# Kernel optimization log

Measured on AMD Instinct MI355X. Metric: run time of the kernel, lower is better.

## Reference

```python
import jax, jax.numpy as jnp
import numpy as np

FEAT_DIM = 64   # C
EMBED_DIM = 64  # E
NUM_HEADS = 4
B, K, H, W = 4, 8, 128, 128


def setup_inputs() -> dict:
    key = jax.random.key(0)
    ks = jax.random.split(key, 24)
    C, E = FEAT_DIM, EMBED_DIM

    def lin_w(k, out_d, in_d):
        return jax.random.normal(k, (out_d, in_d), jnp.float32) * (1.0 / np.sqrt(in_d))

    def lin_b(k, out_d):
        return jax.random.normal(k, (out_d,), jnp.float32) * 0.01

    return {
        "HF_star": jax.random.normal(ks[0], (B, C, H, W), jnp.float32),
        "HF_cands": jax.random.normal(ks[1], (B, K, C, H, W), jnp.float32),
        "Z_cands": jax.random.normal(ks[2], (B, K, C, H, W), jnp.float32),
        "q1_w": lin_w(ks[3], E, C + 2), "q1_b": lin_b(ks[4], E),
        "k1_w": lin_w(ks[5], E, C + 2), "k1_b": lin_b(ks[6], E),
        "v1_w": lin_w(ks[7], E, C), "v1_b": lin_b(ks[8], E),
        "q2_w": lin_w(ks[9], E, C + E + 2), "q2_b": lin_b(ks[10], E),
        "k2_w": lin_w(ks[11], E, C + E + 2), "k2_b": lin_b(ks[12], E),
        "v2_w": lin_w(ks[13], E, C + E), "v2_b": lin_b(ks[14], E),
        "in_proj_w": lin_w(ks[15], 3 * E, E), "in_proj_b": lin_b(ks[16], 3 * E),
        "out_w": lin_w(ks[17], E, E), "out_b": lin_b(ks[18], E),
    }


def _mha(q, k, v, in_proj_w, in_proj_b, out_w, out_b, num_heads):
    # Replicates torch nn.MultiheadAttention with query len 1 per pixel.
    # q: [BN, E], k/v: [BN, K, E]
    E = q.shape[-1]
    d = E // num_heads
    wq, wk, wv = jnp.split(in_proj_w, 3, axis=0)
    bq, bk, bv = jnp.split(in_proj_b, 3, axis=0)
    qh = (q @ wq.T + bq).reshape(-1, num_heads, d)                  # [BN,h,d]
    kh = (k @ wk.T + bk).reshape(k.shape[0], k.shape[1], num_heads, d)  # [BN,K,h,d]
    vh = (v @ wv.T + bv).reshape(v.shape[0], v.shape[1], num_heads, d)
    scale = 1.0 / np.sqrt(d).astype(np.float32)
    scores = jnp.einsum('bhd,bkhd->bhk', qh, kh) * scale            # [BN,h,K]
    attn = jax.nn.softmax(scores, axis=-1)
    out = jnp.einsum('bhk,bkhd->bhd', attn, vh).reshape(-1, E)      # [BN,E]
    return out @ out_w.T + out_b


def reference(HF_star, HF_cands, Z_cands,
              q1_w, q1_b, k1_w, k1_b, v1_w, v1_b,
              q2_w, q2_b, k2_w, k2_b, v2_w, v2_b,
              in_proj_w, in_proj_b, out_w, out_b):
    Bb, C, Hh, Ww = HF_star.shape
    Kk = HF_cands.shape[1]
    N = Hh * Ww
    E = out_w.shape[0]

    i = jnp.linspace(0.0, 1.0, Hh)
    j = jnp.linspace(0.0, 1.0, Ww)
    ig, jg = jnp.meshgrid(i, j, indexing='ij')
    coords = jnp.stack([ig, jg], axis=-1)                            # [H,W,2]

    Qpix = jnp.transpose(HF_star, (0, 2, 3, 1))                      # [B,H,W,C]
    Kc = jnp.transpose(HF_cands, (0, 1, 3, 4, 2))                    # [B,K,H,W,C]
    Vc = jnp.transpose(Z_cands, (0, 1, 3, 4, 2))                     # [B,K,H,W,C]
    coords_q = jnp.broadcast_to(coords, (Bb, Hh, Ww, 2))
    coords_k = jnp.broadcast_to(coords, (Bb, Kk, Hh, Ww, 2))

    # Stage 1 (note: key reshape [B,K,H,W,D] -> [B*N,K,D] matches torch reshape semantics)
    Q1 = jnp.concatenate([Qpix, coords_q], axis=-1).reshape(Bb * N, C + 2)
    K1 = jnp.concatenate([Kc, coords_k], axis=-1).reshape(Bb * N, Kk, C + 2)
    V1 = Vc.reshape(Bb * N, Kk, C)
    q = Q1 @ q1_w.T + q1_b
    k = K1 @ k1_w.T + k1_b
    v = V1 @ v1_w.T + v1_b
    z_star = _mha(q, k, v, in_proj_w, in_proj_b, out_w, out_b, NUM_HEADS)
    z_bhwe = z_star.reshape(Bb, Hh, Ww, E)                           # [B,H,W,E]
    z_k = jnp.broadcast_to(z_bhwe[:, None], (Bb, Kk, Hh, Ww, E))

    # Stage 2
    Q2 = jnp.concatenate([Qpix, z_bhwe, coords_q], axis=-1).reshape(Bb * N, C + E + 2)
    K2 = jnp.concatenate([Kc, z_k, coords_k], axis=-1).reshape(Bb * N, Kk, C + E + 2)
    V2 = jnp.concatenate([Vc, z_k], axis=-1).reshape(Bb * N, Kk, C + E)
    q = Q2 @ q2_w.T + q2_b
    k = K2 @ k2_w.T + k2_b
    v = V2 @ v2_w.T + v2_b
    z_hat = _mha(q, k, v, in_proj_w, in_proj_b, out_w, out_b, NUM_HEADS)
    return jnp.transpose(z_hat.reshape(Bb, Hh, Ww, E), (0, 3, 1, 2))  # [B,E,H,W]
```

## Files before the change

### kernel.cpp

```cpp
#include <hip/hip_runtime.h>
#include <math.h>

#define HWp 16384
#define CH 64
#define KC 8
#define WSTRIDE 136

typedef __attribute__((ext_vector_type(8))) short bf16x8;
typedef __attribute__((ext_vector_type(4))) float f32x4;

#define MFMA(a, b, c) __builtin_amdgcn_mfma_f32_16x16x32_bf16(a, b, c, 0, 0, 0)

__device__ __forceinline__ short f2bf(float f) {
  unsigned u = __float_as_uint(f);
  u += 0x7FFFu + ((u >> 16) & 1u);
  return (short)(u >> 16);
}
__device__ __forceinline__ float bf2f(short s) {
  return __uint_as_float(((unsigned)(unsigned short)s) << 16);
}

__device__ __forceinline__ bf16x8 ldB(const short* __restrict__ W, int nrow, int c0) {
  return *(const bf16x8*)(W + nrow * WSTRIDE + c0);
}
__device__ __forceinline__ bf16x8 ldA_g(const float* __restrict__ base, int c0, int row) {
  bf16x8 f;
#pragma unroll
  for (int j = 0; j < 8; ++j) f[j] = f2bf(base[(size_t)(c0 + j) * HWp + row]);
  return f;
}
__device__ __forceinline__ bf16x8 ldA_z(const short* __restrict__ zrow, int c0) {
  return *(const bf16x8*)(zrow + c0);
}

__global__ void setup_weights(const float* __restrict__ q1w, const float* __restrict__ q1b,
                              const float* __restrict__ k1w, const float* __restrict__ k1b,
                              const float* __restrict__ v1w, const float* __restrict__ v1b,
                              const float* __restrict__ q2w, const float* __restrict__ q2b,
                              const float* __restrict__ k2w, const float* __restrict__ k2b,
                              const float* __restrict__ v2w, const float* __restrict__ v2b,
                              const float* __restrict__ ipw, const float* __restrict__ ipb,
                              const float* __restrict__ ow, short* __restrict__ Wt,
                              float* __restrict__ Bc) {
  int id = blockIdx.y;
  int idx = blockIdx.x * 256 + threadIdx.x;
  if (id == 6) {
    if (idx < 4096) {
      int e = idx >> 6, d = idx & 63;
      Wt[(6 * 64 + e) * WSTRIDE + d] = f2bf(ow[e * 64 + d]);
    }
    return;
  }
  const float* lw; const float* lb; int K, off;
  switch (id) {
    case 0:  lw = q1w; lb = q1b; K = 66;  off = 0;   break;
    case 1:  lw = k1w; lb = k1b; K = 66;  off = 64;  break;
    case 2:  lw = v1w; lb = v1b; K = 64;  off = 128; break;
    case 3:  lw = q2w; lb = q2b; K = 130; off = 0;   break;
    case 4:  lw = k2w; lb = k2b; K = 130; off = 64;  break;
    default: lw = v2w; lb = v2b; K = 128; off = 128; break;
  }
  if (idx < K * 64) {
    int c = idx >> 6, e = idx & 63;
    float s = 0.f;
    for (int f = 0; f < 64; ++f) s += ipw[(off + e) * 64 + f] * lw[f * K + c];
    Wt[(id * 64 + e) * WSTRIDE + c] = f2bf(s);
  } else if (idx < K * 64 + 64) {
    int e = idx - K * 64;
    float s = ipb[off + e];
    for (int f = 0; f < 64; ++f) s += ipw[(off + e) * 64 + f] * lb[f];
    Bc[id * 64 + e] = s;
  }
}

__global__ __launch_bounds__(256) void stage1(const float* __restrict__ HFs,
                                              const float* __restrict__ HFc,
                                              const float* __restrict__ Zc,
                                              const short* __restrict__ Wt,
                                              const float* __restrict__ Bc,
                                              const float* __restrict__ outb,
                                              short* __restrict__ zb) {
  const int t = threadIdx.x;
  const int wv = t >> 6, l = t & 63;
  const int tile = blockIdx.x;
  const int b = tile >> 11;
  const int p0 = (tile & 2047) << 3;
  const int m0 = p0 << 3;
  const int k0 = m0 >> 14;
  const int poff = m0 & (HWp - 1);

  __shared__ float KV[64 * 77];
  __shared__ float QH[8 * 68];
  __shared__ float AO[8 * 68];
  __shared__ float ATT[256];

  const int am = l & 15, kg = l >> 4, n = l & 15;
  const int row0 = wv * 16;

  const short* Wq = Wt + 0 * 64 * WSTRIDE;
  const short* Wk = Wt + 1 * 64 * WSTRIDE;
  const short* Wv = Wt + 2 * 64 * WSTRIDE;
  const short* Wo = Wt + 6 * 64 * WSTRIDE;
  const float* BQ = Bc + 0 * 64;
  const float* BK = Bc + 1 * 64;
  const float* BV = Bc + 2 * 64;

  const float* baseKc = HFc + ((size_t)(b * KC + k0) * CH) * HWp + poff;
  const float* baseZc = Zc + ((size_t)(b * KC + k0) * CH) * HWp + poff;
  const float* baseQ = HFs + (size_t)b * CH * HWp;
  const float inv127 = 1.f / 127.f;

  f32x4 kacc[4];
#pragma unroll
  for (int ct = 0; ct < 4; ++ct) {
    int col = ct * 16 + n;
    float bk = BK[col];
    float wi = bf2f(Wk[col * WSTRIDE + 64]);
    float wj = bf2f(Wk[col * WSTRIDE + 65]);
#pragma unroll
    for (int r = 0; r < 4; ++r) {
      int pp = poff + row0 + kg * 4 + r;
      kacc[ct][r] = bk + (float)(pp >> 7) * inv127 * wi + (float)(pp & 127) * inv127 * wj;
    }
  }
  f32x4 qacc;
  {
    int colq = wv * 16 + n;
    float bq = BQ[colq];
    float wi = bf2f(Wq[colq * WSTRIDE + 64]);
    float wj = bf2f(Wq[colq * WSTRIDE + 65]);
#pragma unroll
    for (int r = 0; r < 4; ++r) {
      int p = p0 + ((kg * 4 + r) & 7);
      qacc[r] = bq + (float)(p >> 7) * inv127 * wi + (float)(p & 127) * inv127 * wj;
    }
  }
#pragma unroll
  for (int ks = 0; ks < 2; ++ks) {
    int c0 = ks * 32 + kg * 8;
    bf16x8 a = ldA_g(baseKc, c0, row0 + am);
#pragma unroll
    for (int ct = 0; ct < 4; ++ct) kacc[ct] = MFMA(a, ldB(Wk, ct * 16 + n, c0), kacc[ct]);
    bf16x8 aq = ldA_g(baseQ, c0, p0 + (am & 7));
    qacc = MFMA(aq, ldB(Wq, wv * 16 + n, c0), qacc);
  }
#pragma unroll
  for (int ct = 0; ct < 4; ++ct)
#pragma unroll
    for (int r = 0; r < 4; ++r)
      KV[(row0 + kg * 4 + r) * 77 + ct * 16 + n] = kacc[ct][r];
#pragma unroll
  for (int r = 0; r < 4; ++r) {
    int m = kg * 4 + r;
    if (m < 8) QH[m * 68 + wv * 16 + n] = qacc[r];
  }
  __syncthreads();

  {
    int p = t >> 5, k = t & 7, h = (t >> 3) & 3;
    const float* qrow = &QH[p * 68 + h * 16];
    const float* krow = &KV[(p * 8 + k) * 77 + h * 16];
    float s = 0.f;
#pragma unroll
    for (int d = 0; d < 16; ++d) s += qrow[d] * krow[d];
    s *= 0.25f;
    float mx = s;
    mx = fmaxf(mx, __shfl_xor(mx, 1));
    mx = fmaxf(mx, __shfl_xor(mx, 2));
    mx = fmaxf(mx, __shfl_xor(mx, 4));
    float e = __expf(s - mx);
    float sum = e;
    sum += __shfl_xor(sum, 1);
    sum += __shfl_xor(sum, 2);
    sum += __shfl_xor(sum, 4);
    ATT[t] = e / sum;
  }
  __syncthreads();

  f32x4 vacc[4];
#pragma unroll
  for (int ct = 0; ct < 4; ++ct) {
    float bv = BV[ct * 16 + n];
#pragma unroll
    for (int r = 0; r < 4; ++r) vacc[ct][r] = bv;
  }
#pragma unroll
  for (int ks = 0; ks < 2; ++ks) {
    int c0 = ks * 32 + kg * 8;
    bf16x8 a = ldA_g(baseZc, c0, row0 + am);
#pragma unroll
    for (int ct = 0; ct < 4; ++ct) vacc[ct] = MFMA(a, ldB(Wv, ct * 16 + n, c0), vacc[ct]);
  }
#pragma unroll
  for (int ct = 0; ct < 4; ++ct)
#pragma unroll
    for (int r = 0; r < 4; ++r)
      KV[(row0 + kg * 4 + r) * 77 + ct * 16 + n] = vacc[ct][r];
  __syncthreads();

  {
    int p = t >> 5, dp = t & 7, h = (t >> 3) & 3;
    int d0 = h * 16 + dp * 2;
    float o0 = 0.f, o1 = 0.f;
#pragma unroll
    for (int k = 0; k < 8; ++k) {
      float a = ATT[(t & ~7) + k];
      const float* vrow = &KV[(p * 8 + k) * 77 + d0];
      o0 += a * vrow[0];
      o1 += a * vrow[1];
    }
    AO[p * 68 + d0] = o0;
    AO[p * 68 + d0 + 1] = o1;
  }
  __syncthreads();

  {
    int colo = wv * 16 + n;
    f32x4 oacc;
    float bo = outb[colo];
#pragma unroll
    for (int r = 0; r < 4; ++r) oacc[r] = bo;
#pragma unroll
    for (int ks = 0; ks < 2; ++ks) {
      int c0 = ks * 32 + kg * 8;
      bf16x8 a;
#pragma unroll
      for (int j = 0; j < 8; ++j) a[j] = f2bf(AO[(am & 7) * 68 + c0 + j]);
      oacc = MFMA(a, ldB(Wo, colo, c0), oacc);
    }
#pragma unroll
    for (int r = 0; r < 4; ++r) {
      int m = kg * 4 + r;
      if (m < 8) zb[((size_t)(b * HWp + p0 + m)) * 64 + colo] = f2bf(oacc[r]);
    }
  }
}

__global__ __launch_bounds__(256) void stage2(const float* __restrict__ HFs,
                                              const float* __restrict__ HFc,
                                              const float* __restrict__ Zc,
                                              const short* __restrict__ Wt,
                                              const float* __restrict__ Bc,
                                              const float* __restrict__ outb,
                                              const short* __restrict__ zb,
                                              float* __restrict__ out) {
  const int t = threadIdx.x;
  const int wv = t >> 6, l = t & 63;
  const int tile = blockIdx.x;
  const int b = tile >> 11;
  const int p0 = (tile & 2047) << 3;
  const int m0 = p0 << 3;
  const int k0 = m0 >> 14;
  const int poff = m0 & (HWp - 1);

  __shared__ float KV[64 * 77];
  __shared__ float QH[8 * 68];
  __shared__ float AO[8 * 68];
  __shared__ float ATT[256];

  const int am = l & 15, kg = l >> 4, n = l & 15;
  const int row0 = wv * 16;

  const short* Wq = Wt + 3 * 64 * WSTRIDE;
  const short* Wk = Wt + 4 * 64 * WSTRIDE;
  const short* Wv = Wt + 5 * 64 * WSTRIDE;
  const short* Wo = Wt + 6 * 64 * WSTRIDE;
  const float* BQ = Bc + 3 * 64;
  const float* BK = Bc + 4 * 64;
  const float* BV = Bc + 5 * 64;

  const float* baseKc = HFc + ((size_t)(b * KC + k0) * CH) * HWp + poff;
  const float* baseZc = Zc + ((size_t)(b * KC + k0) * CH) * HWp + poff;
  const float* baseQ = HFs + (size_t)b * CH * HWp;
  const short* zK = zb + ((size_t)(b * HWp + poff + row0 + am)) * 64;
  const short* zQ = zb + ((size_t)(b * HWp + p0 + (am & 7))) * 64;
  const float inv127 = 1.f / 127.f;

  f32x4 kacc[4];
#pragma unroll
  for (int ct = 0; ct < 4; ++ct) {
    int col = ct * 16 + n;
    float bk = BK[col];
    float wi = bf2f(Wk[col * WSTRIDE + 128]);
    float wj = bf2f(Wk[col * WSTRIDE + 129]);
#pragma unroll
    for (int r = 0; r < 4; ++r) {
      int pp = poff + row0 + kg * 4 + r;
      kacc[ct][r] = bk + (float)(pp >> 7) * inv127 * wi + (float)(pp & 127) * inv127 * wj;
    }
  }
  f32x4 qacc;
  {
    int colq = wv * 16 + n;
    float bq = BQ[colq];
    float wi = bf2f(Wq[colq * WSTRIDE + 128]);
    float wj = bf2f(Wq[colq * WSTRIDE + 129]);
#pragma unroll
    for (int r = 0; r < 4; ++r) {
      int p = p0 + ((kg * 4 + r) & 7);
      qacc[r] = bq + (float)(p >> 7) * inv127 * wi + (float)(p & 127) * inv127 * wj;
    }
  }
#pragma unroll
  for (int ks = 0; ks < 4; ++ks) {
    int c0 = ks * 32 + kg * 8;
    bf16x8 a = (ks < 2) ? ldA_g(baseKc, c0, row0 + am) : ldA_z(zK, c0 - 64);
#pragma unroll
    for (int ct = 0; ct < 4; ++ct) kacc[ct] = MFMA(a, ldB(Wk, ct * 16 + n, c0), kacc[ct]);
    bf16x8 aq = (ks < 2) ? ldA_g(baseQ, c0, p0 + (am & 7)) : ldA_z(zQ, c0 - 64);
    qacc = MFMA(aq, ldB(Wq, wv * 16 + n, c0), qacc);
  }
#pragma unroll
  for (int ct = 0; ct < 4; ++ct)
#pragma unroll
    for (int r = 0; r < 4; ++r)
      KV[(row0 + kg * 4 + r) * 77 + ct * 16 + n] = kacc[ct][r];
#pragma unroll
  for (int r = 0; r < 4; ++r) {
    int m = kg * 4 + r;
    if (m < 8) QH[m * 68 + wv * 16 + n] = qacc[r];
  }
  __syncthreads();

  {
    int p = t >> 5, k = t & 7, h = (t >> 3) & 3;
    const float* qrow = &QH[p * 68 + h * 16];
    const float* krow = &KV[(p * 8 + k) * 77 + h * 16];
    float s = 0.f;
#pragma unroll
    for (int d = 0; d < 16; ++d) s += qrow[d] * krow[d];
    s *= 0.25f;
    float mx = s;
    mx = fmaxf(mx, __shfl_xor(mx, 1));
    mx = fmaxf(mx, __shfl_xor(mx, 2));
    mx = fmaxf(mx, __shfl_xor(mx, 4));
    float e = __expf(s - mx);
    float sum = e;
    sum += __shfl_xor(sum, 1);
    sum += __shfl_xor(sum, 2);
    sum += __shfl_xor(sum, 4);
    ATT[t] = e / sum;
  }
  __syncthreads();

  f32x4 vacc[4];
#pragma unroll
  for (int ct = 0; ct < 4; ++ct) {
    float bv = BV[ct * 16 + n];
#pragma unroll
    for (int r = 0; r < 4; ++r) vacc[ct][r] = bv;
  }
#pragma unroll
  for (int ks = 0; ks < 4; ++ks) {
    int c0 = ks * 32 + kg * 8;
    bf16x8 a = (ks < 2) ? ldA_g(baseZc, c0, row0 + am) : ldA_z(zK, c0 - 64);
#pragma unroll
    for (int ct = 0; ct < 4; ++ct) vacc[ct] = MFMA(a, ldB(Wv, ct * 16 + n, c0), vacc[ct]);
  }
#pragma unroll
  for (int ct = 0; ct < 4; ++ct)
#pragma unroll
    for (int r = 0; r < 4; ++r)
      KV[(row0 + kg * 4 + r) * 77 + ct * 16 + n] = vacc[ct][r];
  __syncthreads();

  {
    int p = t >> 5, dp = t & 7, h = (t >> 3) & 3;
    int d0 = h * 16 + dp * 2;
    float o0 = 0.f, o1 = 0.f;
#pragma unroll
    for (int k = 0; k < 8; ++k) {
      float a = ATT[(t & ~7) + k];
      const float* vrow = &KV[(p * 8 + k) * 77 + d0];
      o0 += a * vrow[0];
      o1 += a * vrow[1];
    }
    AO[p * 68 + d0] = o0;
    AO[p * 68 + d0 + 1] = o1;
  }
  __syncthreads();

  {
    int colo = wv * 16 + n;
    f32x4 oacc;
    float bo = outb[colo];
#pragma unroll
    for (int r = 0; r < 4; ++r) oacc[r] = bo;
#pragma unroll
    for (int ks = 0; ks < 2; ++ks) {
      int c0 = ks * 32 + kg * 8;
      bf16x8 a;
#pragma unroll
      for (int j = 0; j < 8; ++j) a[j] = f2bf(AO[(am & 7) * 68 + c0 + j]);
      oacc = MFMA(a, ldB(Wo, colo, c0), oacc);
    }
#pragma unroll
    for (int r = 0; r < 4; ++r) {
      int m = kg * 4 + r;
      if (m < 8) out[((size_t)(b * 64 + colo)) * HWp + p0 + m] = oacc[r];
    }
  }
}

extern "C" void kernel_launch(void* const* d_in, const int* in_sizes, int n_in,
                              void* d_out, int out_size, void* d_ws, size_t ws_size,
                              hipStream_t stream) {
  const float* HFs = (const float*)d_in[0];
  const float* HFc = (const float*)d_in[1];
  const float* Zc = (const float*)d_in[2];
  const float* q1w = (const float*)d_in[3];  const float* q1b = (const float*)d_in[4];
  const float* k1w = (const float*)d_in[5];  const float* k1b = (const float*)d_in[6];
  const float* v1w = (const float*)d_in[7];  const float* v1b = (const float*)d_in[8];
  const float* q2w = (const float*)d_in[9];  const float* q2b = (const float*)d_in[10];
  const float* k2w = (const float*)d_in[11]; const float* k2b = (const float*)d_in[12];
  const float* v2w = (const float*)d_in[13]; const float* v2b = (const float*)d_in[14];
  const float* ipw = (const float*)d_in[15]; const float* ipb = (const float*)d_in[16];
  const float* ow = (const float*)d_in[17];  const float* ob = (const float*)d_in[18];

  short* Wt = (short*)d_ws;
  float* Bc = (float*)((char*)d_ws + 121856);
  short* zb = (short*)((char*)d_ws + 131072);
  float* out = (float*)d_out;

  dim3 gsetup(33, 7);
  setup_weights<<<gsetup, 256, 0, stream>>>(q1w, q1b, k1w, k1b, v1w, v1b,
                                            q2w, q2b, k2w, k2b, v2w, v2b,
                                            ipw, ipb, ow, Wt, Bc);
  stage1<<<8192, 256, 0, stream>>>(HFs, HFc, Zc, Wt, Bc, ob, zb);
  stage2<<<8192, 256, 0, stream>>>(HFs, HFc, Zc, Wt, Bc, ob, zb, out);
}
```

Before: 541.7 us.

## Compute attention scores and softmax in registers via shuffles, prefetch all inputs upfront

```diff
diff --git a/kernel.cpp b/kernel.cpp
--- a/kernel.cpp
+++ b/kernel.cpp
@@ -19,18 +19,14 @@
 __device__ __forceinline__ float bf2f(short s) {
   return __uint_as_float(((unsigned)(unsigned short)s) << 16);
 }
-
 __device__ __forceinline__ bf16x8 ldB(const short* __restrict__ W, int nrow, int c0) {
   return *(const bf16x8*)(W + nrow * WSTRIDE + c0);
 }
-__device__ __forceinline__ bf16x8 ldA_g(const float* __restrict__ base, int c0, int row) {
-  bf16x8 f;
-#pragma unroll
-  for (int j = 0; j < 8; ++j) f[j] = f2bf(base[(size_t)(c0 + j) * HWp + row]);
-  return f;
-}
-__device__ __forceinline__ bf16x8 ldA_z(const short* __restrict__ zrow, int c0) {
-  return *(const bf16x8*)(zrow + c0);
+__device__ __forceinline__ bf16x8 cvt8(const float* r) {
+  bf16x8 a;
+#pragma unroll
+  for (int j = 0; j < 8; ++j) a[j] = f2bf(r[j]);
+  return a;
 }
 
 __global__ void setup_weights(const float* __restrict__ q1w, const float* __restrict__ q1b,
@@ -80,149 +76,138 @@
                                               const float* __restrict__ Bc,
                                               const float* __restrict__ outb,
                                               short* __restrict__ zb) {
-  const int t = threadIdx.x;
-  const int wv = t >> 6, l = t & 63;
-  const int tile = blockIdx.x;
-  const int b = tile >> 11;
-  const int p0 = (tile & 2047) << 3;
-  const int m0 = p0 << 3;
-  const int k0 = m0 >> 14;
-  const int poff = m0 & (HWp - 1);
-
-  __shared__ float KV[64 * 77];
-  __shared__ float QH[8 * 68];
+  const int t = threadIdx.x, wv = t >> 6, l = t & 63;
+  const int tile = blockIdx.x, b = tile >> 11, p0 = (tile & 2047) << 3;
+  const int m0 = p0 << 3, k0 = m0 >> 14, poff = m0 & (HWp - 1);
+
   __shared__ float AO[8 * 68];
-  __shared__ float ATT[256];
-
-  const int am = l & 15, kg = l >> 4, n = l & 15;
-  const int row0 = wv * 16;
-
-  const short* Wq = Wt + 0 * 64 * WSTRIDE;
-  const short* Wk = Wt + 1 * 64 * WSTRIDE;
+
+  const int am = l & 15, kg = l >> 4;
+  const int row0 = wv << 4;
+  const int c0a = kg * 8;
+  const int rowK = row0 + am;
+  const int pq = p0 + 2 * wv + (am >> 3);
+
+  const short* Wq = Wt;
+  const short* Wk = Wt + 64 * WSTRIDE;
   const short* Wv = Wt + 2 * 64 * WSTRIDE;
   const short* Wo = Wt + 6 * 64 * WSTRIDE;
-  const float* BQ = Bc + 0 * 64;
-  const float* BK = Bc + 1 * 64;
-  const float* BV = Bc + 2 * 64;
+  const float* BQ = Bc;
+  const float* BK = Bc + 64;
+  const float* BV = Bc + 128;
 
   const float* baseKc = HFc + ((size_t)(b * KC + k0) * CH) * HWp + poff;
   const float* baseZc = Zc + ((size_t)(b * KC + k0) * CH) * HWp + poff;
   const float* baseQ = HFs + (size_t)b * CH * HWp;
   const float inv127 = 1.f / 127.f;
 
-  f32x4 kacc[4];
-#pragma unroll
-  for (int ct = 0; ct < 4; ++ct) {
-    int col = ct * 16 + n;
-    float bk = BK[col];
-    float wi = bf2f(Wk[col * WSTRIDE + 64]);
-    float wj = bf2f(Wk[col * WSTRIDE + 65]);
+  float rK[16], rQ[16], rV[16];
+#pragma unroll
+  for (int ks = 0; ks < 2; ++ks)
+#pragma unroll
+    for (int j = 0; j < 8; ++j)
+      rK[ks * 8 + j] = baseKc[(size_t)(ks * 32 + c0a + j) * HWp + rowK];
+#pragma unroll
+  for (int ks = 0; ks < 2; ++ks)
+#pragma unroll
+    for (int j = 0; j < 8; ++j)
+      rQ[ks * 8 + j] = baseQ[(size_t)(ks * 32 + c0a + j) * HWp + pq];
+#pragma unroll
+  for (int ks = 0; ks < 2; ++ks)
+#pragma unroll
+    for (int j = 0; j < 8; ++j)
+      rV[ks * 8 + j] = baseZc[(size_t)(ks * 32 + c0a + j) * HWp + rowK];
+
+  const int pqd = p0 + 2 * wv + (kg >> 1);
+  const float qi = (float)(pqd >> 7) * inv127, qj = (float)(pqd & 127) * inv127;
+  f32x4 kacc[4], qacc[4];
+#pragma unroll
+  for (int ct = 0; ct < 4; ++ct) {
+    int col = ct * 16 + am;
+    float bk = BK[col], wi = bf2f(Wk[col * WSTRIDE + 64]), wj = bf2f(Wk[col * WSTRIDE + 65]);
 #pragma unroll
     for (int r = 0; r < 4; ++r) {
       int pp = poff + row0 + kg * 4 + r;
       kacc[ct][r] = bk + (float)(pp >> 7) * inv127 * wi + (float)(pp & 127) * inv127 * wj;
     }
-  }
-  f32x4 qacc;
+    float bq = BQ[col] + qi * bf2f(Wq[col * WSTRIDE + 64]) + qj * bf2f(Wq[col * WSTRIDE + 65]);
+#pragma unroll
+    for (int r = 0; r < 4; ++r) qacc[ct][r] = bq;
+  }
+#pragma unroll
+  for (int ks = 0; ks < 2; ++ks) {
+    int c0 = ks * 32 + c0a;
+    bf16x8 aK = cvt8(rK + ks * 8), aQ = cvt8(rQ + ks * 8);
+#pragma unroll
+    for (int ct = 0; ct < 4; ++ct) {
+      kacc[ct] = MFMA(aK, ldB(Wk, ct * 16 + am, c0), kacc[ct]);
+      qacc[ct] = MFMA(aQ, ldB(Wq, ct * 16 + am, c0), qacc[ct]);
+    }
+  }
+
+  float sc[4][4];
+#pragma unroll
+  for (int ct = 0; ct < 4; ++ct)
+#pragma unroll
+    for (int r = 0; r < 4; ++r) sc[ct][r] = kacc[ct][r] * qacc[ct][0];
+#pragma unroll
+  for (int m = 1; m < 16; m <<= 1)
+#pragma unroll
+    for (int ct = 0; ct < 4; ++ct)
+#pragma unroll
+      for (int r = 0; r < 4; ++r) sc[ct][r] += __shfl_xor(sc[ct][r], m);
+
+  float aw[4][4];
+#pragma unroll
+  for (int ct = 0; ct < 4; ++ct) {
+    float so[4];
+#pragma unroll
+    for (int r = 0; r < 4; ++r) { sc[ct][r] *= 0.25f; so[r] = __shfl_xor(sc[ct][r], 16); }
+    float mx = fmaxf(fmaxf(fmaxf(sc[ct][0], sc[ct][1]), fmaxf(sc[ct][2], sc[ct][3])),
+                     fmaxf(fmaxf(so[0], so[1]), fmaxf(so[2], so[3])));
+    float e[4], s = 0.f;
+#pragma unroll
+    for (int r = 0; r < 4; ++r) { e[r] = __expf(sc[ct][r] - mx); s += e[r]; }
+#pragma unroll
+    for (int r = 0; r < 4; ++r) s += __expf(so[r] - mx);
+    float inv = 1.0f / s;
+#pragma unroll
+    for (int r = 0; r < 4; ++r) aw[ct][r] = e[r] * inv;
+  }
+
+  f32x4 vacc[4];
+#pragma unroll
+  for (int ct = 0; ct < 4; ++ct) {
+    float bv = BV[ct * 16 + am];
+#pragma unroll
+    for (int r = 0; r < 4; ++r) vacc[ct][r] = bv;
+  }
+#pragma unroll
+  for (int ks = 0; ks < 2; ++ks) {
+    int c0 = ks * 32 + c0a;
+    bf16x8 aV = cvt8(rV + ks * 8);
+#pragma unroll
+    for (int ct = 0; ct < 4; ++ct) vacc[ct] = MFMA(aV, ldB(Wv, ct * 16 + am, c0), vacc[ct]);
+  }
+
+#pragma unroll
+  for (int ct = 0; ct < 4; ++ct) {
+    float po = aw[ct][0] * vacc[ct][0] + aw[ct][1] * vacc[ct][1] +
+               aw[ct][2] * vacc[ct][2] + aw[ct][3] * vacc[ct][3];
+    po += __shfl_xor(po, 16);
+    if ((kg & 1) == 0) AO[(2 * wv + (kg >> 1)) * 68 + ct * 16 + am] = po;
+  }
+  __syncthreads();
+
   {
-    int colq = wv * 16 + n;
-    float bq = BQ[colq];
-    float wi = bf2f(Wq[colq * WSTRIDE + 64]);
-    float wj = bf2f(Wq[colq * WSTRIDE + 65]);
-#pragma unroll
-    for (int r = 0; r < 4; ++r) {
-      int p = p0 + ((kg * 4 + r) & 7);
-      qacc[r] = bq + (float)(p >> 7) * inv127 * wi + (float)(p & 127) * inv127 * wj;
-    }
-  }
-#pragma unroll
-  for (int ks = 0; ks < 2; ++ks) {
-    int c0 = ks * 32 + kg * 8;
-    bf16x8 a = ldA_g(baseKc, c0, row0 + am);
-#pragma unroll
-    for (int ct = 0; ct < 4; ++ct) kacc[ct] = MFMA(a, ldB(Wk, ct * 16 + n, c0), kacc[ct]);
-    bf16x8 aq = ldA_g(baseQ, c0, p0 + (am & 7));
-    qacc = MFMA(aq, ldB(Wq, wv * 16 + n, c0), qacc);
-  }
-#pragma unroll
-  for (int ct = 0; ct < 4; ++ct)
-#pragma unroll
-    for (int r = 0; r < 4; ++r)
-      KV[(row0 + kg * 4 + r) * 77 + ct * 16 + n] = kacc[ct][r];
-#pragma unroll
-  for (int r = 0; r < 4; ++r) {
-    int m = kg * 4 + r;
-    if (m < 8) QH[m * 68 + wv * 16 + n] = qacc[r];
-  }
-  __syncthreads();
-
-  {
-    int p = t >> 5, k = t & 7, h = (t >> 3) & 3;
-    const float* qrow = &QH[p * 68 + h * 16];
-    const float* krow = &KV[(p * 8 + k) * 77 + h * 16];
-    float s = 0.f;
-#pragma unroll
-    for (int d = 0; d < 16; ++d) s += qrow[d] * krow[d];
-    s *= 0.25f;
-    float mx = s;
-    mx = fmaxf(mx, __shfl_xor(mx, 1));
-    mx = fmaxf(mx, __shfl_xor(mx, 2));
-    mx = fmaxf(mx, __shfl_xor(mx, 4));
-    float e = __expf(s - mx);
-    float sum = e;
-    sum += __shfl_xor(sum, 1);
-    sum += __shfl_xor(sum, 2);
-    sum += __shfl_xor(sum, 4);
-    ATT[t] = e / sum;
-  }
-  __syncthreads();
-
-  f32x4 vacc[4];
-#pragma unroll
-  for (int ct = 0; ct < 4; ++ct) {
-    float bv = BV[ct * 16 + n];
-#pragma unroll
-    for (int r = 0; r < 4; ++r) vacc[ct][r] = bv;
-  }
-#pragma unroll
-  for (int ks = 0; ks < 2; ++ks) {
-    int c0 = ks * 32 + kg * 8;
-    bf16x8 a = ldA_g(baseZc, c0, row0 + am);
-#pragma unroll
-    for (int ct = 0; ct < 4; ++ct) vacc[ct] = MFMA(a, ldB(Wv, ct * 16 + n, c0), vacc[ct]);
-  }
-#pragma unroll
-  for (int ct = 0; ct < 4; ++ct)
-#pragma unroll
-    for (int r = 0; r < 4; ++r)
-      KV[(row0 + kg * 4 + r) * 77 + ct * 16 + n] = vacc[ct][r];
-  __syncthreads();
-
-  {
-    int p = t >> 5, dp = t & 7, h = (t >> 3) & 3;
-    int d0 = h * 16 + dp * 2;
-    float o0 = 0.f, o1 = 0.f;
-#pragma unroll
-    for (int k = 0; k < 8; ++k) {
-      float a = ATT[(t & ~7) + k];
-      const float* vrow = &KV[(p * 8 + k) * 77 + d0];
-      o0 += a * vrow[0];
-      o1 += a * vrow[1];
-    }
-    AO[p * 68 + d0] = o0;
-    AO[p * 68 + d0 + 1] = o1;
-  }
-  __syncthreads();
-
-  {
-    int colo = wv * 16 + n;
+    int colo = wv * 16 + am;
     f32x4 oacc;
     float bo = outb[colo];
 #pragma unroll
     for (int r = 0; r < 4; ++r) oacc[r] = bo;
 #pragma unroll
     for (int ks = 0; ks < 2; ++ks) {
-      int c0 = ks * 32 + kg * 8;
+      int c0 = ks * 32 + c0a;
       bf16x8 a;
 #pragma unroll
       for (int j = 0; j < 8; ++j) a[j] = f2bf(AO[(am & 7) * 68 + c0 + j]);
@@ -244,151 +229,147 @@
                                               const float* __restrict__ outb,
                                               const short* __restrict__ zb,
                                               float* __restrict__ out) {
-  const int t = threadIdx.x;
-  const int wv = t >> 6, l = t & 63;
-  const int tile = blockIdx.x;
-  const int b = tile >> 11;
-  const int p0 = (tile & 2047) << 3;
-  const int m0 = p0 << 3;
-  const int k0 = m0 >> 14;
-  const int poff = m0 & (HWp - 1);
-
-  __shared__ float KV[64 * 77];
-  __shared__ float QH[8 * 68];
+  const int t = threadIdx.x, wv = t >> 6, l = t & 63;
+  const int tile = blockIdx.x, b = tile >> 11, p0 = (tile & 2047) << 3;
+  const int m0 = p0 << 3, k0 = m0 >> 14, poff = m0 & (HWp - 1);
+
   __shared__ float AO[8 * 68];
-  __shared__ float ATT[256];
-
-  const int am = l & 15, kg = l >> 4, n = l & 15;
-  const int row0 = wv * 16;
+
+  const int am = l & 15, kg = l >> 4;
+  const int row0 = wv << 4;
+  const int c0a = kg * 8;
+  const int rowK = row0 + am;
+  const int pq = p0 + 2 * wv + (am >> 3);
 
   const short* Wq = Wt + 3 * 64 * WSTRIDE;
   const short* Wk = Wt + 4 * 64 * WSTRIDE;
   const short* Wv = Wt + 5 * 64 * WSTRIDE;
   const short* Wo = Wt + 6 * 64 * WSTRIDE;
-  const float* BQ = Bc + 3 * 64;
-  const float* BK = Bc + 4 * 64;
-  const float* BV = Bc + 5 * 64;
+  const float* BQ = Bc + 192;
+  const float* BK = Bc + 256;
+  const float* BV = Bc + 320;
 
   const float* baseKc = HFc + ((size_t)(b * KC + k0) * CH) * HWp + poff;
   const float* baseZc = Zc + ((size_t)(b * KC + k0) * CH) * HWp + poff;
   const float* baseQ = HFs + (size_t)b * CH * HWp;
-  const short* zK = zb + ((size_t)(b * HWp + poff + row0 + am)) * 64;
-  const short* zQ = zb + ((size_t)(b * HWp + p0 + (am & 7))) * 64;
+  const short* zK = zb + ((size_t)(b * HWp + poff + rowK)) * 64;
+  const short* zQ = zb + ((size_t)(b * HWp + pq)) * 64;
   const float inv127 = 1.f / 127.f;
 
-  f32x4 kacc[4];
-#pragma unroll
-  for (int ct = 0; ct < 4; ++ct) {
-    int col = ct * 16 + n;
-    float bk = BK[col];
-    float wi = bf2f(Wk[col * WSTRIDE + 128]);
-    float wj = bf2f(Wk[col * WSTRIDE + 129]);
+  float rK[16], rQ[16], rV[16];
+  bf16x8 zKf[2], zQf[2];
+#pragma unroll
+  for (int ks = 0; ks < 2; ++ks)
+#pragma unroll
+    for (int j = 0; j < 8; ++j)
+      rK[ks * 8 + j] = baseKc[(size_t)(ks * 32 + c0a + j) * HWp + rowK];
+#pragma unroll
+  for (int ks = 0; ks < 2; ++ks)
+#pragma unroll
+    for (int j = 0; j < 8; ++j)
+      rQ[ks * 8 + j] = baseQ[(size_t)(ks * 32 + c0a + j) * HWp + pq];
+#pragma unroll
+  for (int ks = 0; ks < 2; ++ks)
+#pragma unroll
+    for (int j = 0; j < 8; ++j)
+      rV[ks * 8 + j] = baseZc[(size_t)(ks * 32 + c0a + j) * HWp + rowK];
+#pragma unroll
+  for (int i = 0; i < 2; ++i) {
+    zKf[i] = *(const bf16x8*)(zK + i * 32 + c0a);
+    zQf[i] = *(const bf16x8*)(zQ + i * 32 + c0a);
+  }
+
+  const int pqd = p0 + 2 * wv + (kg >> 1);
+  const float qi = (float)(pqd >> 7) * inv127, qj = (float)(pqd & 127) * inv127;
+  f32x4 kacc[4], qacc[4];
+#pragma unroll
+  for (int ct = 0; ct < 4; ++ct) {
+    int col = ct * 16 + am;
+    float bk = BK[col], wi = bf2f(Wk[col * WSTRIDE + 128]), wj = bf2f(Wk[col * WSTRIDE + 129]);
 #pragma unroll
     for (int r = 0; r < 4; ++r) {
       int pp = poff + row0 + kg * 4 + r;
       kacc[ct][r] = bk + (float)(pp >> 7) * inv127 * wi + (float)(pp & 127) * inv127 * wj;
     }
-  }
-  f32x4 qacc;
+    float bq = BQ[col] + qi * bf2f(Wq[col * WSTRIDE + 128]) + qj * bf2f(Wq[col * WSTRIDE + 129]);
+#pragma unroll
+    for (int r = 0; r < 4; ++r) qacc[ct][r] = bq;
+  }
+#pragma unroll
+  for (int ks = 0; ks < 4; ++ks) {
+    int c0 = ks * 32 + c0a;
+    bf16x8 aK = (ks < 2) ? cvt8(rK + ks * 8) : zKf[ks - 2];
+    bf16x8 aQ = (ks < 2) ? cvt8(rQ + ks * 8) : zQf[ks - 2];
+#pragma unroll
+    for (int ct = 0; ct < 4; ++ct) {
+      kacc[ct] = MFMA(aK, ldB(Wk, ct * 16 + am, c0), kacc[ct]);
+      qacc[ct] = MFMA(aQ, ldB(Wq, ct * 16 + am, c0), qacc[ct]);
+    }
+  }
+
+  float sc[4][4];
+#pragma unroll
+  for (int ct = 0; ct < 4; ++ct)
+#pragma unroll
+    for (int r = 0; r < 4; ++r) sc[ct][r] = kacc[ct][r] * qacc[ct][0];
+#pragma unroll
+  for (int m = 1; m < 16; m <<= 1)
+#pragma unroll
+    for (int ct = 0; ct < 4; ++ct)
+#pragma unroll
+      for (int r = 0; r < 4; ++r) sc[ct][r] += __shfl_xor(sc[ct][r], m);
+
+  float aw[4][4];
+#pragma unroll
+  for (int ct = 0; ct < 4; ++ct) {
+    float so[4];
+#pragma unroll
+    for (int r = 0; r < 4; ++r) { sc[ct][r] *= 0.25f; so[r] = __shfl_xor(sc[ct][r], 16); }
+    float mx = fmaxf(fmaxf(fmaxf(sc[ct][0], sc[ct][1]), fmaxf(sc[ct][2], sc[ct][3])),
+                     fmaxf(fmaxf(so[0], so[1]), fmaxf(so[2], so[3])));
+    float e[4], s = 0.f;
+#pragma unroll
+    for (int r = 0; r < 4; ++r) { e[r] = __expf(sc[ct][r] - mx); s += e[r]; }
+#pragma unroll
+    for (int r = 0; r < 4; ++r) s += __expf(so[r] - mx);
+    float inv = 1.0f / s;
+#pragma unroll
+    for (int r = 0; r < 4; ++r) aw[ct][r] = e[r] * inv;
+  }
+
+  f32x4 vacc[4];
+#pragma unroll
+  for (int ct = 0; ct < 4; ++ct) {
+    float bv = BV[ct * 16 + am];
+#pragma unroll
+    for (int r = 0; r < 4; ++r) vacc[ct][r] = bv;
+  }
+#pragma unroll
+  for (int ks = 0; ks < 4; ++ks) {
+    int c0 = ks * 32 + c0a;
+    bf16x8 aV = (ks < 2) ? cvt8(rV + ks * 8) : zKf[ks - 2];
+#pragma unroll
+    for (int ct = 0; ct < 4; ++ct) vacc[ct] = MFMA(aV, ldB(Wv, ct * 16 + am, c0), vacc[ct]);
+  }
+
+#pragma unroll
+  for (int ct = 0; ct < 4; ++ct) {
+    float po = aw[ct][0] * vacc[ct][0] + aw[ct][1] * vacc[ct][1] +
+               aw[ct][2] * vacc[ct][2] + aw[ct][3] * vacc[ct][3];
+    po += __shfl_xor(po, 16);
+    if ((kg & 1) == 0) AO[(2 * wv + (kg >> 1)) * 68 + ct * 16 + am] = po;
+  }
+  __syncthreads();
+
   {
-    int colq = wv * 16 + n;
-    float bq = BQ[colq];
-    float wi = bf2f(Wq[colq * WSTRIDE + 128]);
-    float wj = bf2f(Wq[colq * WSTRIDE + 129]);
-#pragma unroll
-    for (int r = 0; r < 4; ++r) {
-      int p = p0 + ((kg * 4 + r) & 7);
-      qacc[r] = bq + (float)(p >> 7) * inv127 * wi + (float)(p & 127) * inv127 * wj;
-    }
-  }
-#pragma unroll
-  for (int ks = 0; ks < 4; ++ks) {
-    int c0 = ks * 32 + kg * 8;
-    bf16x8 a = (ks < 2) ? ldA_g(baseKc, c0, row0 + am) : ldA_z(zK, c0 - 64);
-#pragma unroll
-    for (int ct = 0; ct < 4; ++ct) kacc[ct] = MFMA(a, ldB(Wk, ct * 16 + n, c0), kacc[ct]);
-    bf16x8 aq = (ks < 2) ? ldA_g(baseQ, c0, p0 + (am & 7)) : ldA_z(zQ, c0 - 64);
-    qacc = MFMA(aq, ldB(Wq, wv * 16 + n, c0), qacc);
-  }
-#pragma unroll
-  for (int ct = 0; ct < 4; ++ct)
-#pragma unroll
-    for (int r = 0; r < 4; ++r)
-      KV[(row0 + kg * 4 + r) * 77 + ct * 16 + n] = kacc[ct][r];
-#pragma unroll
-  for (int r = 0; r < 4; ++r) {
-    int m = kg * 4 + r;
-    if (m < 8) QH[m * 68 + wv * 16 + n] = qacc[r];
-  }
-  __syncthreads();
-
-  {
-    int p = t >> 5, k = t & 7, h = (t >> 3) & 3;
-    const float* qrow = &QH[p * 68 + h * 16];
-    const float* krow = &KV[(p * 8 + k) * 77 + h * 16];
-    float s = 0.f;
-#pragma unroll
-    for (int d = 0; d < 16; ++d) s += qrow[d] * krow[d];
-    s *= 0.25f;
-    float mx = s;
-    mx = fmaxf(mx, __shfl_xor(mx, 1));
-    mx = fmaxf(mx, __shfl_xor(mx, 2));
-    mx = fmaxf(mx, __shfl_xor(mx, 4));
-    float e = __expf(s - mx);
-    float sum = e;
-    sum += __shfl_xor(sum, 1);
-    sum += __shfl_xor(sum, 2);
-    sum += __shfl_xor(sum, 4);
-    ATT[t] = e / sum;
-  }
-  __syncthreads();
-
-  f32x4 vacc[4];
-#pragma unroll
-  for (int ct = 0; ct < 4; ++ct) {
-    float bv = BV[ct * 16 + n];
-#pragma unroll
-    for (int r = 0; r < 4; ++r) vacc[ct][r] = bv;
-  }
-#pragma unroll
-  for (int ks = 0; ks < 4; ++ks) {
-    int c0 = ks * 32 + kg * 8;
-    bf16x8 a = (ks < 2) ? ldA_g(baseZc, c0, row0 + am) : ldA_z(zK, c0 - 64);
-#pragma unroll
-    for (int ct = 0; ct < 4; ++ct) vacc[ct] = MFMA(a, ldB(Wv, ct * 16 + n, c0), vacc[ct]);
-  }
-#pragma unroll
-  for (int ct = 0; ct < 4; ++ct)
-#pragma unroll
-    for (int r = 0; r < 4; ++r)
-      KV[(row0 + kg * 4 + r) * 77 + ct * 16 + n] = vacc[ct][r];
-  __syncthreads();
-
-  {
-    int p = t >> 5, dp = t & 7, h = (t >> 3) & 3;
-    int d0 = h * 16 + dp * 2;
-    float o0 = 0.f, o1 = 0.f;
-#pragma unroll
-    for (int k = 0; k < 8; ++k) {
-      float a = ATT[(t & ~7) + k];
-      const float* vrow = &KV[(p * 8 + k) * 77 + d0];
-      o0 += a * vrow[0];
-      o1 += a * vrow[1];
-    }
-    AO[p * 68 + d0] = o0;
-    AO[p * 68 + d0 + 1] = o1;
-  }
-  __syncthreads();
-
-  {
-    int colo = wv * 16 + n;
+    int colo = wv * 16 + am;
     f32x4 oacc;
     float bo = outb[colo];
 #pragma unroll
     for (int r = 0; r < 4; ++r) oacc[r] = bo;
 #pragma unroll
     for (int ks = 0; ks < 2; ++ks) {
-      int c0 = ks * 32 + kg * 8;
+      int c0 = ks * 32 + c0a;
       bf16x8 a;
 #pragma unroll
       for (int j = 0; j < 8; ++j) a[j] = f2bf(AO[(am & 7) * 68 + c0 + j]);
```

Measured after the change: 603.7 us. 1.11x slower.
